# Optimization experiments

Measured on AMD Instinct MI355X. Metric: run time of the kernel, lower is better.

The kernel has to match this reference:

```python
import jax, jax.numpy as jnp
import numpy as np

T_TOTAL = 64          # ODE time horizon (frames)
OBS_RANGE = 32        # int(T * obs) with obs = 0.5
B, C, V = 512, 64, 25 # (N*M) batch, base_channel, num joints


def make_pe(length, d):
    # sinusoidal positional encoding, matching ODEFunc.init_pe -> (length, d)
    pos = jnp.arange(length, dtype=jnp.float32)[:, None]
    div = jnp.exp(jnp.arange(0, d, 2, dtype=jnp.float32) * (-np.log(10000.0) / d))
    pe = jnp.zeros((length, d), dtype=jnp.float32)
    pe = pe.at[:, 0::2].set(jnp.sin(pos * div))
    pe = pe.at[:, 1::2].set(jnp.cos(pos * div))
    return pe


def setup_inputs() -> dict:
    key = jax.random.key(0)
    ks = jax.random.split(key, 10)
    s = 0.1  # keep tanh chain unsaturated
    return {
        "z": jax.random.normal(ks[0], (B, C, T_TOTAL, V), jnp.float32),
        "A": jax.random.normal(ks[1], (V, V), jnp.float32) * s,
        "w1": jax.random.normal(ks[2], (C, C), jnp.float32) * s,
        "b1": jax.random.normal(ks[3], (C,), jnp.float32) * s,
        "w2": jax.random.normal(ks[4], (C, C), jnp.float32) * s,
        "b2": jax.random.normal(ks[5], (C,), jnp.float32) * s,
        "w3": jax.random.normal(ks[6], (C, C), jnp.float32) * s,
        "b3": jax.random.normal(ks[7], (C,), jnp.float32) * s,
        "w4": jax.random.normal(ks[8], (C, C), jnp.float32) * s,
        "b4": jax.random.normal(ks[9], (C,), jnp.float32) * s,
    }


def _ode_f(x, pe_t, A, w1, b1, w2, b2, w3, b3, w4, b4):
    # ODEFunc.forward: x + pe; (A @ x -> 1x1 conv -> tanh) x3; proj
    # x: (b, c, t, v); pe_t: (c,); A: (v, u); w*: (out_c, in_c)
    x = x + pe_t[None, :, None, None]
    x = jnp.einsum('vu,bctu->bctv', A, x)
    x = jnp.tanh(jnp.einsum('oc,bctv->botv', w1, x) + b1[None, :, None, None])
    x = jnp.einsum('vu,bctu->bctv', A, x)
    x = jnp.tanh(jnp.einsum('oc,bctv->botv', w2, x) + b2[None, :, None, None])
    x = jnp.einsum('vu,bctu->bctv', A, x)
    x = jnp.tanh(jnp.einsum('oc,bctv->botv', w3, x) + b3[None, :, None, None])
    x = jnp.einsum('oc,bctv->botv', w4, x) + b4[None, :, None, None]
    return x


def _rk4_step(y, pe0, pe1, params):
    # torchdiffeq 'rk4' fixed-grid step (three-eighths rule), dt = 1.
    # ODEFunc truncates t via int(t.item()): stages at t, t+1/3, t+2/3 use pe0, stage at t+1 uses pe1.
    f = lambda x, p: _ode_f(x, p, *params)
    k1 = f(y, pe0)
    k2 = f(y + k1 / 3.0, pe0)
    k3 = f(y + (k2 - k1 / 3.0), pe0)
    k4 = f(y + (k1 - k2 + k3), pe1)
    return y + (k1 + 3.0 * (k2 + k3) + k4) / 8.0


def reference(z, A, w1, b1, w2, b2, w3, b3, w4, b4):
    # InfoGCN.extrapolate (training=True): per-frame one-step RK4 for the
    # observed range, then a sequential RK4 rollout for the predicted range.
    pe = make_pe(T_TOTAL, C)
    params = (A, w1, b1, w2, b2, w3, b3, w4, b4)

    # observed frames: every step integrates t: 0 -> 1, independent per frame
    # -> vectorize the 32 per-frame ODE solves as one batched step.
    z_hat = _rk4_step(z[:, :, :OBS_RANGE, :], pe[0], pe[1], params)  # (B,C,32,V)

    # prediction: sequential rollout from frame OBS_RANGE-1 over t = 0..n_pred
    n_pred = T_TOTAL - OBS_RANGE
    z0 = z[:, :, OBS_RANGE - 1:OBS_RANGE, :]  # (B, C, 1, V)

    def body(y, pes):
        p0, p1 = pes
        y1 = _rk4_step(y, p0, p1, params)
        return y1, y1[:, :, 0, :]

    _, preds = jax.lax.scan(body, z0, (pe[:n_pred], pe[1:n_pred + 1]))
    preds = jnp.moveaxis(preds, 0, 2)  # (B, C, n_pred, V)

    return jnp.concatenate([z_hat, preds], axis=2)  # (B, C, T_TOTAL, V)
```

## Files before the change

### kernel.cpp

```cpp
#include <hip/hip_runtime.h>
#include <math.h>

#define CC 64
#define VV 25
#define VP 26
#define T_TOTAL 64
#define OBS 32
#define BATCH 512
#define NTHREADS 256
#define TV (T_TOTAL * VV)

__device__ __forceinline__ float tanh_fast(float x) {
    float t = fminf(fmaxf(2.0f * x, -30.0f), 30.0f);
    float e = __expf(t);
    return (e - 1.0f) / (e + 1.0f);
}

__device__ __forceinline__ void amul(float* __restrict__ dst, const float* __restrict__ srcb,
                                     const float* __restrict__ As, const float* __restrict__ rsA,
                                     const float* __restrict__ pe, int tid)
{
    int c = tid >> 2, vs = tid & 3;
    float acc[7];
    float pec = (pe != nullptr) ? pe[c] : 0.0f;
    #pragma unroll
    for (int j = 0; j < 7; ++j) {
        int v = vs + 4 * j;
        acc[j] = (pe != nullptr && v < VV) ? pec * rsA[v] : 0.0f;
    }
    #pragma unroll
    for (int u = 0; u < VV; ++u) {
        float x = srcb[c * VP + u];
        #pragma unroll
        for (int j = 0; j < 7; ++j) {
            int v = vs + 4 * j;
            if (v < VV) acc[j] = fmaf(x, As[v * VP + u], acc[j]);
        }
    }
    #pragma unroll
    for (int j = 0; j < 7; ++j) {
        int v = vs + 4 * j;
        if (v < VV) dst[c * VP + v] = acc[j];
    }
    __syncthreads();
}

__device__ __forceinline__ void wmul(float* __restrict__ dst, const float* __restrict__ srcb,
                                     const float* __restrict__ Wg, const float* __restrict__ Bg,
                                     bool dotanh, int tid)
{
    int o = tid >> 2, vs = tid & 3;
    float acc[7];
    float b = Bg[o];
    #pragma unroll
    for (int j = 0; j < 7; ++j) acc[j] = b;
    #pragma unroll 8
    for (int cc = 0; cc < CC; ++cc) {
        float w = Wg[o * CC + cc];
        #pragma unroll
        for (int j = 0; j < 7; ++j) {
            int v = vs + 4 * j;
            if (v < VV) acc[j] = fmaf(w, srcb[cc * VP + v], acc[j]);
        }
    }
    #pragma unroll
    for (int j = 0; j < 7; ++j) {
        int v = vs + 4 * j;
        if (v < VV) {
            float r = acc[j];
            dst[o * VP + v] = dotanh ? tanh_fast(r) : r;
        }
    }
    __syncthreads();
}

__device__ __forceinline__ void ode_f(float* out, float* s0, float* s1,
                                      const float* As, const float* rsA, const float* pe0,
                                      const float* W1, const float* B1,
                                      const float* W2, const float* B2,
                                      const float* W3, const float* B3,
                                      const float* W4, const float* B4, int tid)
{
    amul(s1, s0, As, rsA, pe0, tid);
    wmul(s0, s1, W1, B1, true, tid);
    amul(s1, s0, As, rsA, nullptr, tid);
    wmul(s0, s1, W2, B2, true, tid);
    amul(s1, s0, As, rsA, nullptr, tid);
    wmul(s0, s1, W3, B3, true, tid);
    wmul(out, s0, W4, B4, false, tid);
}

__global__ void __launch_bounds__(NTHREADS)
rk4_kernel(const float* __restrict__ src, float* __restrict__ dst,
           const float* __restrict__ Ag, const float* __restrict__ pe,
           const float* __restrict__ W1, const float* __restrict__ B1,
           const float* __restrict__ W2, const float* __restrict__ B2,
           const float* __restrict__ W3, const float* __restrict__ B3,
           const float* __restrict__ W4, const float* __restrict__ B4,
           int nt, int src_t0, int dst_t0, int pe_row)
{
    __shared__ float y[CC * VP], k1[CC * VP], k2[CC * VP], k3[CC * VP];
    __shared__ float s0[CC * VP], s1[CC * VP];
    __shared__ float As[VV * VP], rsA[VV];

    int tid = threadIdx.x;
    int blk = blockIdx.x;
    int b  = blk / nt;
    int tt = blk - b * nt;
    int t_src = src_t0 + tt;
    int t_dst = dst_t0 + tt;

    const float* pe0 = pe + pe_row * CC;
    const float* pe1 = pe0 + CC;

    for (int i = tid; i < VV * VV; i += NTHREADS) {
        int v = i / VV, u = i - v * VV;
        As[v * VP + u] = Ag[i];
    }
    __syncthreads();
    if (tid < VV) {
        float s = 0.0f;
        #pragma unroll
        for (int u = 0; u < VV; ++u) s += As[tid * VP + u];
        rsA[tid] = s;
    }

    const float* srcp = src + (size_t)b * CC * TV + (size_t)t_src * VV;
    for (int i = tid; i < CC * VV; i += NTHREADS) {
        int c = i / VV, v = i - c * VV;
        float val = srcp[(size_t)c * TV + v];
        y[c * VP + v]  = val;
        s0[c * VP + v] = val;
    }
    __syncthreads();

    ode_f(k1, s0, s1, As, rsA, pe0, W1, B1, W2, B2, W3, B3, W4, B4, tid);

    for (int i = tid; i < CC * VV; i += NTHREADS) {
        int c = i / VV, v = i - c * VV; int id = c * VP + v;
        s0[id] = y[id] + k1[id] * (1.0f / 3.0f);
    }
    __syncthreads();
    ode_f(k2, s0, s1, As, rsA, pe0, W1, B1, W2, B2, W3, B3, W4, B4, tid);

    for (int i = tid; i < CC * VV; i += NTHREADS) {
        int c = i / VV, v = i - c * VV; int id = c * VP + v;
        s0[id] = y[id] - k1[id] * (1.0f / 3.0f) + k2[id];
    }
    __syncthreads();
    ode_f(k3, s0, s1, As, rsA, pe0, W1, B1, W2, B2, W3, B3, W4, B4, tid);

    for (int i = tid; i < CC * VV; i += NTHREADS) {
        int c = i / VV, v = i - c * VV; int id = c * VP + v;
        float a = k1[id], bb = k2[id], cc2 = k3[id];
        s0[id] = y[id] + a - bb + cc2;
        k1[id] = a + 3.0f * (bb + cc2);
    }
    __syncthreads();
    ode_f(k2, s0, s1, As, rsA, pe1, W1, B1, W2, B2, W3, B3, W4, B4, tid);

    float* dstp = dst + (size_t)b * CC * TV + (size_t)t_dst * VV;
    for (int i = tid; i < CC * VV; i += NTHREADS) {
        int c = i / VV, v = i - c * VV; int id = c * VP + v;
        dstp[(size_t)c * TV + v] = y[id] + (k1[id] + k2[id]) * 0.125f;
    }
}

__global__ void pe_kernel(float* __restrict__ pe) {
    int idx = blockIdx.x * blockDim.x + threadIdx.x;
    if (idx >= T_TOTAL * CC) return;
    int t = idx >> 6, c = idx & 63;
    int i2 = c & ~1;
    float div = expf((float)i2 * (-logf(10000.0f) / (float)CC));
    float arg = (float)t * div;
    pe[idx] = (c & 1) ? cosf(arg) : sinf(arg);
}

extern "C" void kernel_launch(void* const* d_in, const int* in_sizes, int n_in,
                              void* d_out, int out_size, void* d_ws, size_t ws_size,
                              hipStream_t stream) {
    const float* z  = (const float*)d_in[0];
    const float* A  = (const float*)d_in[1];
    const float* w1 = (const float*)d_in[2];
    const float* b1 = (const float*)d_in[3];
    const float* w2 = (const float*)d_in[4];
    const float* b2 = (const float*)d_in[5];
    const float* w3 = (const float*)d_in[6];
    const float* b3 = (const float*)d_in[7];
    const float* w4 = (const float*)d_in[8];
    const float* b4 = (const float*)d_in[9];
    float* out = (float*)d_out;
    float* pe  = (float*)d_ws;

    pe_kernel<<<(T_TOTAL * CC + 255) / 256, 256, 0, stream>>>(pe);

    rk4_kernel<<<BATCH * OBS, NTHREADS, 0, stream>>>(
        z, out, A, pe, w1, b1, w2, b2, w3, b3, w4, b4,
        OBS, 0, 0, 0);

    for (int i = 0; i < 32; ++i) {
        const float* srcp = (i == 0) ? z : out;
        rk4_kernel<<<BATCH, NTHREADS, 0, stream>>>(
            srcp, out, A, pe, w1, b1, w2, b2, w3, b3, w4, b4,
            1, 31 + i, 32 + i, i);
    }
}
```

Measured before the change: 8.287 ms.

## Fuse observed and rollout RK4 into one persistent kernel with register-resident state

Replaces the 33 separate RK4 launches with a single kernel. The first 512 blocks each run the 32-step sequential rollout for one batch item, and the remaining blocks handle the independent observed frames. The RK4 state and stage derivatives now stay in registers, threads move to 128 with two output channels each, float4 shared-memory loads are used, and a transposed intermediate layout replaces the padded one. This removes launch overhead and global round-trips between steps, but the long scan blocks become a serial tail that the short blocks must hide.

New measurement: 21.61 ms. +160.8%, slower.

```diff
diff --git a/kernel.cpp b/kernel.cpp
--- a/kernel.cpp
+++ b/kernel.cpp
@@ -1,14 +1,10 @@
 #include <hip/hip_runtime.h>
 #include <math.h>
 
-#define CC 64
-#define VV 25
-#define VP 26
-#define T_TOTAL 64
-#define OBS 32
-#define BATCH 512
-#define NTHREADS 256
-#define TV (T_TOTAL * VV)
+#define NTH 128
+#define XW 28
+#define CP 68
+#define NV 28
 
 __device__ __forceinline__ float tanh_fast(float x) {
     float t = fminf(fmaxf(2.0f * x, -30.0f), 30.0f);
@@ -16,162 +12,204 @@
     return (e - 1.0f) / (e + 1.0f);
 }
 
-__device__ __forceinline__ void amul(float* __restrict__ dst, const float* __restrict__ srcb,
-                                     const float* __restrict__ As, const float* __restrict__ rsA,
-                                     const float* __restrict__ pe, int tid)
-{
-    int c = tid >> 2, vs = tid & 3;
-    float acc[7];
-    float pec = (pe != nullptr) ? pe[c] : 0.0f;
-    #pragma unroll
-    for (int j = 0; j < 7; ++j) {
-        int v = vs + 4 * j;
-        acc[j] = (pe != nullptr && v < VV) ? pec * rsA[v] : 0.0f;
-    }
-    #pragma unroll
-    for (int u = 0; u < VV; ++u) {
-        float x = srcb[c * VP + u];
-        #pragma unroll
-        for (int j = 0; j < 7; ++j) {
-            int v = vs + 4 * j;
-            if (v < VV) acc[j] = fmaf(x, As[v * VP + u], acc[j]);
-        }
-    }
-    #pragma unroll
-    for (int j = 0; j < 7; ++j) {
-        int v = vs + 4 * j;
-        if (v < VV) dst[c * VP + v] = acc[j];
-    }
-    __syncthreads();
-}
-
-__device__ __forceinline__ void wmul(float* __restrict__ dst, const float* __restrict__ srcb,
-                                     const float* __restrict__ Wg, const float* __restrict__ Bg,
-                                     bool dotanh, int tid)
-{
-    int o = tid >> 2, vs = tid & 3;
-    float acc[7];
-    float b = Bg[o];
-    #pragma unroll
-    for (int j = 0; j < 7; ++j) acc[j] = b;
-    #pragma unroll 8
-    for (int cc = 0; cc < CC; ++cc) {
-        float w = Wg[o * CC + cc];
-        #pragma unroll
-        for (int j = 0; j < 7; ++j) {
-            int v = vs + 4 * j;
-            if (v < VV) acc[j] = fmaf(w, srcb[cc * VP + v], acc[j]);
-        }
-    }
-    #pragma unroll
-    for (int j = 0; j < 7; ++j) {
-        int v = vs + 4 * j;
-        if (v < VV) {
-            float r = acc[j];
-            dst[o * VP + v] = dotanh ? tanh_fast(r) : r;
-        }
-    }
-    __syncthreads();
-}
-
-__device__ __forceinline__ void ode_f(float* out, float* s0, float* s1,
-                                      const float* As, const float* rsA, const float* pe0,
-                                      const float* W1, const float* B1,
-                                      const float* W2, const float* B2,
-                                      const float* W3, const float* B3,
-                                      const float* W4, const float* B4, int tid)
-{
-    amul(s1, s0, As, rsA, pe0, tid);
-    wmul(s0, s1, W1, B1, true, tid);
-    amul(s1, s0, As, rsA, nullptr, tid);
-    wmul(s0, s1, W2, B2, true, tid);
-    amul(s1, s0, As, rsA, nullptr, tid);
-    wmul(s0, s1, W3, B3, true, tid);
-    wmul(out, s0, W4, B4, false, tid);
-}
-
-__global__ void __launch_bounds__(NTHREADS)
-rk4_kernel(const float* __restrict__ src, float* __restrict__ dst,
-           const float* __restrict__ Ag, const float* __restrict__ pe,
-           const float* __restrict__ W1, const float* __restrict__ B1,
-           const float* __restrict__ W2, const float* __restrict__ B2,
-           const float* __restrict__ W3, const float* __restrict__ B3,
-           const float* __restrict__ W4, const float* __restrict__ B4,
-           int nt, int src_t0, int dst_t0, int pe_row)
-{
-    __shared__ float y[CC * VP], k1[CC * VP], k2[CC * VP], k3[CC * VP];
-    __shared__ float s0[CC * VP], s1[CC * VP];
-    __shared__ float As[VV * VP], rsA[VV];
+__device__ __forceinline__ void amul(const float* __restrict__ X, float* __restrict__ T,
+                                     const float* __restrict__ As, const float* rsAj,
+                                     float pec0, float pec1, int o0, int o1, int vs)
+{
+    float a0[7], a1[7];
+    #pragma unroll
+    for (int j = 0; j < 7; ++j) { a0[j] = pec0 * rsAj[j]; a1[j] = pec1 * rsAj[j]; }
+    const float* x0p = X + o0 * XW;
+    const float* x1p = X + o1 * XW;
+    #pragma unroll
+    for (int ub = 0; ub < 7; ++ub) {
+        float4 x0 = *(const float4*)(x0p + 4 * ub);
+        float4 x1 = *(const float4*)(x1p + 4 * ub);
+        #pragma unroll
+        for (int j = 0; j < 7; ++j) {
+            float4 a = *(const float4*)(As + (vs + 4 * j) * XW + 4 * ub);
+            a0[j] = fmaf(x0.x, a.x, fmaf(x0.y, a.y, fmaf(x0.z, a.z, fmaf(x0.w, a.w, a0[j]))));
+            a1[j] = fmaf(x1.x, a.x, fmaf(x1.y, a.y, fmaf(x1.z, a.z, fmaf(x1.w, a.w, a1[j]))));
+        }
+    }
+    #pragma unroll
+    for (int j = 0; j < 7; ++j) {
+        int v = vs + 4 * j;
+        T[v * CP + o0] = a0[j];
+        T[v * CP + o1] = a1[j];
+    }
+}
+
+template<int OUT>
+__device__ __forceinline__ void wmul(const float* __restrict__ T, float* __restrict__ Xo,
+                                     float* __restrict__ To, const float* __restrict__ Wg,
+                                     float b0, float b1, int o0, int o1, int vs,
+                                     float* k0, float* k1)
+{
+    float a0[7], a1[7];
+    #pragma unroll
+    for (int j = 0; j < 7; ++j) { a0[j] = b0; a1[j] = b1; }
+    const float* w0p = Wg + o0 * 64;
+    const float* w1p = Wg + o1 * 64;
+    #pragma unroll
+    for (int cb = 0; cb < 16; ++cb) {
+        float4 w0 = *(const float4*)(w0p + 4 * cb);
+        float4 w1 = *(const float4*)(w1p + 4 * cb);
+        #pragma unroll
+        for (int j = 0; j < 7; ++j) {
+            float4 t = *(const float4*)(T + (vs + 4 * j) * CP + 4 * cb);
+            a0[j] = fmaf(w0.x, t.x, fmaf(w0.y, t.y, fmaf(w0.z, t.z, fmaf(w0.w, t.w, a0[j]))));
+            a1[j] = fmaf(w1.x, t.x, fmaf(w1.y, t.y, fmaf(w1.z, t.z, fmaf(w1.w, t.w, a1[j]))));
+        }
+    }
+    #pragma unroll
+    for (int j = 0; j < 7; ++j) {
+        int v = vs + 4 * j;
+        if (OUT == 0)      { Xo[o0 * XW + v] = tanh_fast(a0[j]); Xo[o1 * XW + v] = tanh_fast(a1[j]); }
+        else if (OUT == 1) { To[v * CP + o0] = tanh_fast(a0[j]); To[v * CP + o1] = tanh_fast(a1[j]); }
+        else               { k0[j] = a0[j]; k1[j] = a1[j]; }
+    }
+}
+
+__device__ __forceinline__ void ode_f(float* X, float* Ta, float* Tb, const float* As,
+    const float* rsAj, float pec0, float pec1,
+    const float* W1, float b10, float b11, const float* W2, float b20, float b21,
+    const float* W3, float b30, float b31, const float* W4, float b40, float b41,
+    int o0, int o1, int vs, float* k0, float* k1)
+{
+    amul(X, Ta, As, rsAj, pec0, pec1, o0, o1, vs);
+    __syncthreads();
+    wmul<0>(Ta, X, nullptr, W1, b10, b11, o0, o1, vs, nullptr, nullptr);
+    amul(X, Tb, As, rsAj, 0.f, 0.f, o0, o1, vs);
+    __syncthreads();
+    wmul<0>(Tb, X, nullptr, W2, b20, b21, o0, o1, vs, nullptr, nullptr);
+    amul(X, Ta, As, rsAj, 0.f, 0.f, o0, o1, vs);
+    __syncthreads();
+    wmul<1>(Ta, nullptr, Tb, W3, b30, b31, o0, o1, vs, nullptr, nullptr);
+    __syncthreads();
+    wmul<2>(Tb, nullptr, nullptr, W4, b40, b41, o0, o1, vs, k0, k1);
+}
+
+__global__ void __launch_bounds__(NTH, 3)
+rk4_both(const float* __restrict__ z, float* __restrict__ out,
+         const float* __restrict__ Ag, const float* __restrict__ pe,
+         const float* __restrict__ W1, const float* __restrict__ B1,
+         const float* __restrict__ W2, const float* __restrict__ B2,
+         const float* __restrict__ W3, const float* __restrict__ B3,
+         const float* __restrict__ W4, const float* __restrict__ B4)
+{
+    __shared__ float X[64 * XW];
+    __shared__ float Ta[NV * CP];
+    __shared__ float Tb[NV * CP];
+    __shared__ float As[NV * XW];
 
     int tid = threadIdx.x;
+    int oq = tid >> 2, vs = tid & 3;
+    int o0 = oq, o1 = oq + 32;
+
     int blk = blockIdx.x;
-    int b  = blk / nt;
-    int tt = blk - b * nt;
-    int t_src = src_t0 + tt;
-    int t_dst = dst_t0 + tt;
-
-    const float* pe0 = pe + pe_row * CC;
-    const float* pe1 = pe0 + CC;
-
-    for (int i = tid; i < VV * VV; i += NTHREADS) {
-        int v = i / VV, u = i - v * VV;
-        As[v * VP + u] = Ag[i];
-    }
-    __syncthreads();
-    if (tid < VV) {
-        float s = 0.0f;
-        #pragma unroll
-        for (int u = 0; u < VV; ++u) s += As[tid * VP + u];
-        rsA[tid] = s;
-    }
-
-    const float* srcp = src + (size_t)b * CC * TV + (size_t)t_src * VV;
-    for (int i = tid; i < CC * VV; i += NTHREADS) {
-        int c = i / VV, v = i - c * VV;
-        float val = srcp[(size_t)c * TV + v];
-        y[c * VP + v]  = val;
-        s0[c * VP + v] = val;
-    }
-    __syncthreads();
-
-    ode_f(k1, s0, s1, As, rsA, pe0, W1, B1, W2, B2, W3, B3, W4, B4, tid);
-
-    for (int i = tid; i < CC * VV; i += NTHREADS) {
-        int c = i / VV, v = i - c * VV; int id = c * VP + v;
-        s0[id] = y[id] + k1[id] * (1.0f / 3.0f);
-    }
-    __syncthreads();
-    ode_f(k2, s0, s1, As, rsA, pe0, W1, B1, W2, B2, W3, B3, W4, B4, tid);
-
-    for (int i = tid; i < CC * VV; i += NTHREADS) {
-        int c = i / VV, v = i - c * VV; int id = c * VP + v;
-        s0[id] = y[id] - k1[id] * (1.0f / 3.0f) + k2[id];
-    }
-    __syncthreads();
-    ode_f(k3, s0, s1, As, rsA, pe0, W1, B1, W2, B2, W3, B3, W4, B4, tid);
-
-    for (int i = tid; i < CC * VV; i += NTHREADS) {
-        int c = i / VV, v = i - c * VV; int id = c * VP + v;
-        float a = k1[id], bb = k2[id], cc2 = k3[id];
-        s0[id] = y[id] + a - bb + cc2;
-        k1[id] = a + 3.0f * (bb + cc2);
-    }
-    __syncthreads();
-    ode_f(k2, s0, s1, As, rsA, pe1, W1, B1, W2, B2, W3, B3, W4, B4, tid);
-
-    float* dstp = dst + (size_t)b * CC * TV + (size_t)t_dst * VV;
-    for (int i = tid; i < CC * VV; i += NTHREADS) {
-        int c = i / VV, v = i - c * VV; int id = c * VP + v;
-        dstp[(size_t)c * TV + v] = y[id] + (k1[id] + k2[id]) * 0.125f;
+    bool scan = (blk < 512);
+    int b, t_src, nsteps;
+    if (scan) { b = blk; t_src = 31; nsteps = 32; }
+    else      { int q = blk - 512; b = q >> 5; t_src = q & 31; nsteps = 1; }
+
+    for (int i = tid; i < NV * XW; i += NTH) As[i] = 0.f;
+    __syncthreads();
+    for (int i = tid; i < 25 * 25; i += NTH) { int v = i / 25, u = i - v * 25; As[v * XW + u] = Ag[i]; }
+    __syncthreads();
+
+    float rsAj[7];
+    #pragma unroll
+    for (int j = 0; j < 7; ++j) {
+        float s = 0.f;
+        #pragma unroll
+        for (int ub = 0; ub < 7; ++ub) {
+            float4 a = *(const float4*)(As + (vs + 4 * j) * XW + 4 * ub);
+            s += a.x + a.y + a.z + a.w;
+        }
+        rsAj[j] = s;
+    }
+
+    float b10 = B1[o0], b11 = B1[o1], b20 = B2[o0], b21 = B2[o1];
+    float b30 = B3[o0], b31 = B3[o1], b40 = B4[o0], b41 = B4[o1];
+
+    const float* zb = z + (size_t)b * 64 * 64 * 25;
+    float* outb = out + (size_t)b * 64 * 64 * 25;
+    float y0[7], y1[7];
+    #pragma unroll
+    for (int j = 0; j < 7; ++j) {
+        int v = vs + 4 * j;
+        y0[j] = (v < 25) ? zb[((size_t)o0 * 64 + t_src) * 25 + v] : 0.f;
+        y1[j] = (v < 25) ? zb[((size_t)o1 * 64 + t_src) * 25 + v] : 0.f;
+    }
+    #pragma unroll
+    for (int j = 0; j < 7; ++j) {
+        int v = vs + 4 * j;
+        X[o0 * XW + v] = y0[j];
+        X[o1 * XW + v] = y1[j];
+    }
+
+    for (int s = 0; s < nsteps; ++s) {
+        int pr = scan ? s : 0;
+        float pe00 = pe[pr * 64 + o0], pe01 = pe[pr * 64 + o1];
+        float pe10 = pe[(pr + 1) * 64 + o0], pe11 = pe[(pr + 1) * 64 + o1];
+
+        float ka0[7], ka1[7], kb0[7], kb1[7], kc0[7], kc1[7];
+
+        ode_f(X, Ta, Tb, As, rsAj, pe00, pe01, W1, b10, b11, W2, b20, b21,
+              W3, b30, b31, W4, b40, b41, o0, o1, vs, ka0, ka1);
+        #pragma unroll
+        for (int j = 0; j < 7; ++j) {
+            int v = vs + 4 * j;
+            X[o0 * XW + v] = y0[j] + ka0[j] * (1.f / 3.f);
+            X[o1 * XW + v] = y1[j] + ka1[j] * (1.f / 3.f);
+        }
+        ode_f(X, Ta, Tb, As, rsAj, pe00, pe01, W1, b10, b11, W2, b20, b21,
+              W3, b30, b31, W4, b40, b41, o0, o1, vs, kb0, kb1);
+        #pragma unroll
+        for (int j = 0; j < 7; ++j) {
+            int v = vs + 4 * j;
+            X[o0 * XW + v] = y0[j] - ka0[j] * (1.f / 3.f) + kb0[j];
+            X[o1 * XW + v] = y1[j] - ka1[j] * (1.f / 3.f) + kb1[j];
+        }
+        ode_f(X, Ta, Tb, As, rsAj, pe00, pe01, W1, b10, b11, W2, b20, b21,
+              W3, b30, b31, W4, b40, b41, o0, o1, vs, kc0, kc1);
+        #pragma unroll
+        for (int j = 0; j < 7; ++j) {
+            int v = vs + 4 * j;
+            X[o0 * XW + v] = y0[j] + ka0[j] - kb0[j] + kc0[j];
+            X[o1 * XW + v] = y1[j] + ka1[j] - kb1[j] + kc1[j];
+            ka0[j] = ka0[j] + 3.f * (kb0[j] + kc0[j]);
+            ka1[j] = ka1[j] + 3.f * (kb1[j] + kc1[j]);
+        }
+        ode_f(X, Ta, Tb, As, rsAj, pe10, pe11, W1, b10, b11, W2, b20, b21,
+              W3, b30, b31, W4, b40, b41, o0, o1, vs, kb0, kb1);
+
+        int t_dst = scan ? (32 + s) : t_src;
+        #pragma unroll
+        for (int j = 0; j < 7; ++j) {
+            int v = vs + 4 * j;
+            float n0 = y0[j] + (ka0[j] + kb0[j]) * 0.125f;
+            float n1 = y1[j] + (ka1[j] + kb1[j]) * 0.125f;
+            y0[j] = n0; y1[j] = n1;
+            if (v < 25) {
+                outb[((size_t)o0 * 64 + t_dst) * 25 + v] = n0;
+                outb[((size_t)o1 * 64 + t_dst) * 25 + v] = n1;
+            }
+            if (s + 1 < nsteps) {
+                X[o0 * XW + v] = n0;
+                X[o1 * XW + v] = n1;
+            }
+        }
     }
 }
 
 __global__ void pe_kernel(float* __restrict__ pe) {
     int idx = blockIdx.x * blockDim.x + threadIdx.x;
-    if (idx >= T_TOTAL * CC) return;
+    if (idx >= 64 * 64) return;
     int t = idx >> 6, c = idx & 63;
     int i2 = c & ~1;
-    float div = expf((float)i2 * (-logf(10000.0f) / (float)CC));
+    float div = expf((float)i2 * (-logf(10000.0f) / 64.0f));
     float arg = (float)t * div;
     pe[idx] = (c & 1) ? cosf(arg) : sinf(arg);
 }
@@ -192,16 +230,8 @@
     float* out = (float*)d_out;
     float* pe  = (float*)d_ws;
 
-    pe_kernel<<<(T_TOTAL * CC + 255) / 256, 256, 0, stream>>>(pe);
-
-    rk4_kernel<<<BATCH * OBS, NTHREADS, 0, stream>>>(
-        z, out, A, pe, w1, b1, w2, b2, w3, b3, w4, b4,
-        OBS, 0, 0, 0);
-
-    for (int i = 0; i < 32; ++i) {
-        const float* srcp = (i == 0) ? z : out;
-        rk4_kernel<<<BATCH, NTHREADS, 0, stream>>>(
-            srcp, out, A, pe, w1, b1, w2, b2, w3, b3, w4, b4,
-            1, 31 + i, 32 + i, i);
-    }
-}
+    pe_kernel<<<16, 256, 0, stream>>>(pe);
+
+    rk4_both<<<512 + 512 * 32, NTH, 0, stream>>>(
+        z, out, A, pe, w1, b1, w2, b2, w3, b3, w4, b4);
+}
```
